# Kernel optimization log

Hardware: AMD Instinct MI355X
Metric: run time of the kernel (lower is better)

The kernel has to match this reference:

```python
import jax, jax.numpy as jnp
import numpy as np

QUEST_DIM = 768
C, X, Y = 2048, 19, 19
B = 64

def setup_inputs() -> dict:
    key = jax.random.key(0)
    k1, k2, k3, k4 = jax.random.split(key, 4)
    text_fts = jax.random.normal(k1, (B, QUEST_DIM), dtype=jnp.float32)
    img_fts = jax.random.normal(k2, (B, C, X, Y), dtype=jnp.float32)
    # Linear params (PyTorch nn.Linear: y = x @ W.T + b)
    bound = 1.0 / np.sqrt(QUEST_DIM)
    W = jax.random.uniform(k3, (C, QUEST_DIM), minval=-bound, maxval=bound, dtype=jnp.float32)
    b = jax.random.uniform(k4, (C,), minval=-bound, maxval=bound, dtype=jnp.float32)
    return {"text_fts": text_fts, "img_fts": img_fts, "W": W, "b": b}

def reference(text_fts, img_fts, W, b):
    batch = text_fts.shape[0]
    q = text_fts @ W.T + b                      # [B, C]
    img_flat = img_fts.reshape(batch, C, X * Y) # [B, C, S]
    sims = jnp.einsum('bc,bcs->bs', q, img_flat)  # dot over channel dim
    weights = jax.nn.softmax(sims, axis=1)        # softmax over spatial locations
    final_ans = jnp.einsum('bcs,bs->bc', img_flat, weights)  # weighted pooling
    return final_ans
```

## Files before the change

### kernel.cpp

```cpp
#include <hip/hip_runtime.h>
#include <math.h>

#define Bsz  64
#define Cch  2048
#define Kdim 768
#define Ssp  361

__global__ __launch_bounds__(256) void k_qgemm(
    const float* __restrict__ text, const float* __restrict__ W,
    const float* __restrict__ bias, float* __restrict__ qT)
{
    const int lane = threadIdx.x & 63;
    const int wv   = threadIdx.x >> 6;
    const int c0   = blockIdx.x * 8 + wv * 2;

    const float4* wA = (const float4*)(W + (size_t)c0 * Kdim);
    const float4* wB = (const float4*)(W + (size_t)(c0 + 1) * Kdim);
    const float4 a0 = wA[lane*3+0], a1 = wA[lane*3+1], a2 = wA[lane*3+2];
    const float4 b0 = wB[lane*3+0], b1 = wB[lane*3+1], b2 = wB[lane*3+2];
    const float biasA = bias[c0], biasB = bias[c0 + 1];

    for (int b = 0; b < Bsz; b++) {
        const float4* t = (const float4*)(text + (size_t)b * Kdim);
        const float4 t0 = t[lane*3+0], t1 = t[lane*3+1], t2 = t[lane*3+2];
        float r0 = a0.x*t0.x + a0.y*t0.y + a0.z*t0.z + a0.w*t0.w
                 + a1.x*t1.x + a1.y*t1.y + a1.z*t1.z + a1.w*t1.w
                 + a2.x*t2.x + a2.y*t2.y + a2.z*t2.z + a2.w*t2.w;
        float r1 = b0.x*t0.x + b0.y*t0.y + b0.z*t0.z + b0.w*t0.w
                 + b1.x*t1.x + b1.y*t1.y + b1.z*t1.z + b1.w*t1.w
                 + b2.x*t2.x + b2.y*t2.y + b2.z*t2.z + b2.w*t2.w;
        #pragma unroll
        for (int off = 32; off; off >>= 1) {
            r0 += __shfl_xor(r0, off);
            r1 += __shfl_xor(r1, off);
        }
        if (lane == 0) {
            qT[(size_t)c0 * Bsz + b]       = r0 + biasA;
            qT[(size_t)(c0 + 1) * Bsz + b] = r1 + biasB;
        }
    }
}

__global__ __launch_bounds__(384) void k_sims(
    const float* __restrict__ img, const float* __restrict__ qT,
    float* __restrict__ sims_part)
{
    const int b  = blockIdx.x;
    const int cg = blockIdx.y;
    const int tid = threadIdx.x;

    __shared__ float qL[128];
    if (tid < 128) qL[tid] = qT[(size_t)(cg * 128 + tid) * Bsz + b];
    __syncthreads();

    if (tid < Ssp) {
        const float* base = img + ((size_t)b * Cch + (size_t)cg * 128) * Ssp + tid;
        float acc = 0.f;
        #pragma unroll 8
        for (int c = 0; c < 128; c++)
            acc += qL[c] * base[(size_t)c * Ssp];
        sims_part[((size_t)b * 16 + cg) * Ssp + tid] = acc;
    }
}

__global__ __launch_bounds__(256) void k_pool(
    const float* __restrict__ img, const float* __restrict__ sims_part,
    float* __restrict__ out)
{
    const int b   = blockIdx.x;
    const int cg  = blockIdx.y;
    const int tid = threadIdx.x;
    const int lane = tid & 63;
    const int wv   = tid >> 6;

    __shared__ float w[Ssp];
    __shared__ float red[4];
    __shared__ float outL[64];

    float s0 = -1e30f, s1 = -1e30f;
    if (tid < Ssp) {
        float a = 0.f;
        #pragma unroll
        for (int g = 0; g < 16; g++)
            a += sims_part[((size_t)b * 16 + g) * Ssp + tid];
        s0 = a;
    }
    if (tid + 256 < Ssp) {
        float a = 0.f;
        #pragma unroll
        for (int g = 0; g < 16; g++)
            a += sims_part[((size_t)b * 16 + g) * Ssp + tid + 256];
        s1 = a;
    }

    float m = fmaxf(s0, s1);
    #pragma unroll
    for (int off = 32; off; off >>= 1) m = fmaxf(m, __shfl_xor(m, off));
    if (lane == 0) red[wv] = m;
    __syncthreads();
    m = fmaxf(fmaxf(red[0], red[1]), fmaxf(red[2], red[3]));

    const float e0 = (tid < Ssp)       ? __expf(s0 - m) : 0.f;
    const float e1 = (tid + 256 < Ssp) ? __expf(s1 - m) : 0.f;
    if (tid < Ssp)       w[tid]       = e0;
    if (tid + 256 < Ssp) w[tid + 256] = e1;
    float l = e0 + e1;
    #pragma unroll
    for (int off = 32; off; off >>= 1) l += __shfl_xor(l, off);
    __syncthreads();
    if (lane == 0) red[wv] = l;
    __syncthreads();
    const float inv = 1.f / (red[0] + red[1] + red[2] + red[3]);

    for (int c = wv; c < 64; c += 4) {
        const float* base = img + ((size_t)b * Cch + (size_t)cg * 64 + c) * Ssp;
        float p = 0.f;
        #pragma unroll
        for (int j = 0; j < 5; j++)
            p += base[lane + 64 * j] * w[lane + 64 * j];
        if (lane + 320 < Ssp)
            p += base[lane + 320] * w[lane + 320];
        #pragma unroll
        for (int off = 32; off; off >>= 1) p += __shfl_xor(p, off);
        if (lane == 0) outL[c] = p;
    }
    __syncthreads();
    if (tid < 64)
        out[(size_t)b * Cch + (size_t)cg * 64 + tid] = outL[tid] * inv;
}

extern "C" void kernel_launch(void* const* d_in, const int* in_sizes, int n_in,
                              void* d_out, int out_size, void* d_ws, size_t ws_size,
                              hipStream_t stream) {
    const float* text = (const float*)d_in[0];
    const float* img  = (const float*)d_in[1];
    const float* W    = (const float*)d_in[2];
    const float* bias = (const float*)d_in[3];
    float* out = (float*)d_out;

    float* qT        = (float*)d_ws;
    float* sims_part = qT + (size_t)Cch * Bsz;

    k_qgemm<<<dim3(Cch / 8), 256, 0, stream>>>(text, W, bias, qT);
    k_sims <<<dim3(Bsz, 16), 384, 0, stream>>>(img, qT, sims_part);
    k_pool <<<dim3(Bsz, 32), 256, 0, stream>>>(img, sims_part, out);
}
```

Measured before the change: 349.5 us.

## Split q GEMM over batch chunks and compute softmax weights once per batch

The q projection kernel now launches a 2D grid, with each block handling 16 batch rows instead of all 64. This raises parallelism from 256 blocks to 1024. A new small kernel reduces the partial similarities and computes normalized softmax weights once per batch row. Previously each of the 32 pooling blocks per batch redid the 16-way partial-sum read and the softmax. The trade-off is an extra kernel launch and a workspace round trip, in exchange for less redundant reduction work in the pooling kernel.

```diff
diff --git a/kernel.cpp b/kernel.cpp
--- a/kernel.cpp
+++ b/kernel.cpp
@@ -13,22 +13,23 @@
     const int lane = threadIdx.x & 63;
     const int wv   = threadIdx.x >> 6;
     const int c0   = blockIdx.x * 8 + wv * 2;
+    const int b0   = blockIdx.y * 16;
 
     const float4* wA = (const float4*)(W + (size_t)c0 * Kdim);
     const float4* wB = (const float4*)(W + (size_t)(c0 + 1) * Kdim);
     const float4 a0 = wA[lane*3+0], a1 = wA[lane*3+1], a2 = wA[lane*3+2];
-    const float4 b0 = wB[lane*3+0], b1 = wB[lane*3+1], b2 = wB[lane*3+2];
+    const float4 b0v = wB[lane*3+0], b1v = wB[lane*3+1], b2v = wB[lane*3+2];
     const float biasA = bias[c0], biasB = bias[c0 + 1];
 
-    for (int b = 0; b < Bsz; b++) {
+    for (int b = b0; b < b0 + 16; b++) {
         const float4* t = (const float4*)(text + (size_t)b * Kdim);
         const float4 t0 = t[lane*3+0], t1 = t[lane*3+1], t2 = t[lane*3+2];
         float r0 = a0.x*t0.x + a0.y*t0.y + a0.z*t0.z + a0.w*t0.w
                  + a1.x*t1.x + a1.y*t1.y + a1.z*t1.z + a1.w*t1.w
                  + a2.x*t2.x + a2.y*t2.y + a2.z*t2.z + a2.w*t2.w;
-        float r1 = b0.x*t0.x + b0.y*t0.y + b0.z*t0.z + b0.w*t0.w
-                 + b1.x*t1.x + b1.y*t1.y + b1.z*t1.z + b1.w*t1.w
-                 + b2.x*t2.x + b2.y*t2.y + b2.z*t2.z + b2.w*t2.w;
+        float r1 = b0v.x*t0.x + b0v.y*t0.y + b0v.z*t0.z + b0v.w*t0.w
+                 + b1v.x*t1.x + b1v.y*t1.y + b1v.z*t1.z + b1v.w*t1.w
+                 + b2v.x*t2.x + b2v.y*t2.y + b2v.z*t2.z + b2v.w*t2.w;
         #pragma unroll
         for (int off = 32; off; off >>= 1) {
             r0 += __shfl_xor(r0, off);
@@ -63,8 +64,49 @@
     }
 }
 
+__global__ __launch_bounds__(384) void k_wts(
+    const float* __restrict__ sims_part, float* __restrict__ wts)
+{
+    const int b   = blockIdx.x;
+    const int tid = threadIdx.x;
+    const int lane = tid & 63;
+    const int wv   = tid >> 6;
+
+    __shared__ float red[6];
+
+    float s0 = -1e30f;
+    if (tid < Ssp) {
+        float a = 0.f;
+        #pragma unroll
+        for (int g = 0; g < 16; g++)
+            a += sims_part[((size_t)b * 16 + g) * Ssp + tid];
+        s0 = a;
+    }
+
+    float m = s0;
+    #pragma unroll
+    for (int off = 32; off; off >>= 1) m = fmaxf(m, __shfl_xor(m, off));
+    if (lane == 0) red[wv] = m;
+    __syncthreads();
+    m = red[0];
+    #pragma unroll
+    for (int w = 1; w < 6; w++) m = fmaxf(m, red[w]);
+    __syncthreads();
+
+    const float e0 = (tid < Ssp) ? __expf(s0 - m) : 0.f;
+    float l = e0;
+    #pragma unroll
+    for (int off = 32; off; off >>= 1) l += __shfl_xor(l, off);
+    if (lane == 0) red[wv] = l;
+    __syncthreads();
+    l = red[0] + red[1] + red[2] + red[3] + red[4] + red[5];
+
+    if (tid < Ssp)
+        wts[(size_t)b * Ssp + tid] = e0 / l;
+}
+
 __global__ __launch_bounds__(256) void k_pool(
-    const float* __restrict__ img, const float* __restrict__ sims_part,
+    const float* __restrict__ img, const float* __restrict__ wts,
     float* __restrict__ out)
 {
     const int b   = blockIdx.x;
@@ -74,43 +116,11 @@
     const int wv   = tid >> 6;
 
     __shared__ float w[Ssp];
-    __shared__ float red[4];
     __shared__ float outL[64];
 
-    float s0 = -1e30f, s1 = -1e30f;
-    if (tid < Ssp) {
-        float a = 0.f;
-        #pragma unroll
-        for (int g = 0; g < 16; g++)
-            a += sims_part[((size_t)b * 16 + g) * Ssp + tid];
-        s0 = a;
-    }
-    if (tid + 256 < Ssp) {
-        float a = 0.f;
-        #pragma unroll
-        for (int g = 0; g < 16; g++)
-            a += sims_part[((size_t)b * 16 + g) * Ssp + tid + 256];
-        s1 = a;
-    }
-
-    float m = fmaxf(s0, s1);
-    #pragma unroll
-    for (int off = 32; off; off >>= 1) m = fmaxf(m, __shfl_xor(m, off));
-    if (lane == 0) red[wv] = m;
+    if (tid < Ssp)       w[tid]       = wts[(size_t)b * Ssp + tid];
+    if (tid + 256 < Ssp) w[tid + 256] = wts[(size_t)b * Ssp + tid + 256];
     __syncthreads();
-    m = fmaxf(fmaxf(red[0], red[1]), fmaxf(red[2], red[3]));
-
-    const float e0 = (tid < Ssp)       ? __expf(s0 - m) : 0.f;
-    const float e1 = (tid + 256 < Ssp) ? __expf(s1 - m) : 0.f;
-    if (tid < Ssp)       w[tid]       = e0;
-    if (tid + 256 < Ssp) w[tid + 256] = e1;
-    float l = e0 + e1;
-    #pragma unroll
-    for (int off = 32; off; off >>= 1) l += __shfl_xor(l, off);
-    __syncthreads();
-    if (lane == 0) red[wv] = l;
-    __syncthreads();
-    const float inv = 1.f / (red[0] + red[1] + red[2] + red[3]);
 
     for (int c = wv; c < 64; c += 4) {
         const float* base = img + ((size_t)b * Cch + (size_t)cg * 64 + c) * Ssp;
@@ -126,7 +136,7 @@
     }
     __syncthreads();
     if (tid < 64)
-        out[(size_t)b * Cch + (size_t)cg * 64 + tid] = outL[tid] * inv;
+        out[(size_t)b * Cch + (size_t)cg * 64 + tid] = outL[tid];
 }
 
 extern "C" void kernel_launch(void* const* d_in, const int* in_sizes, int n_in,
@@ -140,8 +150,10 @@
 
     float* qT        = (float*)d_ws;
     float* sims_part = qT + (size_t)Cch * Bsz;
+    float* wts       = sims_part + (size_t)Bsz * 16 * Ssp;
 
-    k_qgemm<<<dim3(Cch / 8), 256, 0, stream>>>(text, W, bias, qT);
+    k_qgemm<<<dim3(256, 4), 256, 0, stream>>>(text, W, bias, qT);
     k_sims <<<dim3(Bsz, 16), 384, 0, stream>>>(img, qT, sims_part);
-    k_pool <<<dim3(Bsz, 32), 256, 0, stream>>>(img, sims_part, out);
+    k_wts  <<<dim3(Bsz),     384, 0, stream>>>(sims_part, wts);
+    k_pool <<<dim3(Bsz, 32), 256, 0, stream>>>(img, wts, out);
 }
```

New measurement: 318.7 us. 1.1x faster.
